# Kernel optimization log

Hardware: AMD Instinct MI355X
Metric: run time of the kernel (lower is better)

The kernel has to match this reference:

```python
import jax, jax.numpy as jnp
import numpy as np

NUM_GRAPHS = 1000


def _gine_conv(x, src, dst, edge_attr, w_e, b_e, w1, b1, w2, b2):
    # GINEConv (eps=0): out = nn(x + sum_{j->i} relu(x_j + lin_edge(e_ji)))
    e = edge_attr @ w_e + b_e                      # [E, F]
    m = jax.nn.relu(x[src] + e)                    # [E, F] per-edge message
    agg = jnp.zeros_like(x).at[dst].add(m)         # [N, F] scatter-add to targets
    h = x + agg
    h = jax.nn.relu(h @ w1 + b1)
    h = jax.nn.relu(h @ w2 + b2)
    return h


def _segment_softmax(scores, seg, num_segments):
    m = jax.ops.segment_max(scores, seg, num_segments=num_segments)
    z = jnp.exp(scores - m[seg])
    s = jax.ops.segment_sum(z, seg, num_segments=num_segments)
    return z / s[seg]


def setup_inputs() -> dict:
    key = jax.random.key(0)
    ks = jax.random.split(key, 16)
    N, E, F_IN, H, ED = 100000, 1600000, 9, 64, 1

    x = jax.random.normal(ks[0], (N, F_IN), dtype=jnp.float32)
    edge_index = jax.random.randint(ks[1], (2, E), 0, N, dtype=jnp.int32)
    edge_attr = jax.random.normal(ks[2], (E, ED), dtype=jnp.float32)
    batch = jnp.sort(jax.random.randint(ks[3], (N,), 0, NUM_GRAPHS, dtype=jnp.int32))
    B_total = jax.random.uniform(ks[4], (NUM_GRAPHS,), dtype=jnp.float32)

    def lin(k, fi, fo):
        k1, k2 = jax.random.split(k)
        bound = 1.0 / np.sqrt(fi)
        w = jax.random.uniform(k1, (fi, fo), minval=-bound, maxval=bound, dtype=jnp.float32)
        b = jax.random.uniform(k2, (fo,), minval=-bound, maxval=bound, dtype=jnp.float32)
        return w, b

    we1, be1 = lin(ks[5], ED, F_IN)    # conv1 edge projection -> in_channels
    w11, b11 = lin(ks[6], F_IN, H)
    w12, b12 = lin(ks[7], H, H)
    we2, be2 = lin(ks[8], ED, H)       # conv2 edge projection
    w21, b21 = lin(ks[9], H, H)
    w22, b22 = lin(ks[10], H, H)
    wr1, br1 = lin(ks[11], H, H // 2)
    wr2, br2 = lin(ks[12], H // 2, 1)

    return {"x": x, "edge_index": edge_index, "edge_attr": edge_attr,
            "batch": batch, "B_total": B_total,
            "we1": we1, "be1": be1, "w11": w11, "b11": b11, "w12": w12, "b12": b12,
            "we2": we2, "be2": be2, "w21": w21, "b21": b21, "w22": w22, "b22": b22,
            "wr1": wr1, "br1": br1, "wr2": wr2, "br2": br2}


def reference(x, edge_index, edge_attr, batch, B_total,
              we1, be1, w11, b11, w12, b12,
              we2, be2, w21, b21, w22, b22,
              wr1, br1, wr2, br2):
    src, dst = edge_index[0], edge_index[1]
    h = _gine_conv(x, src, dst, edge_attr, we1, be1, w11, b11, w12, b12)
    h = _gine_conv(h, src, dst, edge_attr, we2, be2, w21, b21, w22, b22)
    raw = (jax.nn.relu(h @ wr1 + br1) @ wr2 + br2)[:, 0]   # [N]
    alloc_probs = _segment_softmax(raw, batch, NUM_GRAPHS)
    return alloc_probs * B_total[batch]
```

## Files before the change

### kernel.cpp

```cpp
#include <hip/hip_runtime.h>
#include <float.h>

__global__ void deg_rank_kernel(const int* __restrict__ dst, int* __restrict__ deg,
                                int* __restrict__ rank, int E) {
  int j = blockIdx.x * blockDim.x + threadIdx.x;
  if (j < E) rank[j] = atomicAdd(&deg[dst[j]], 1);
}

__global__ void scan_pass1(const int* __restrict__ deg, int* __restrict__ blocksum, int N) {
  __shared__ int sdata[1024];
  int i = blockIdx.x * 1024 + threadIdx.x;
  sdata[threadIdx.x] = (i < N) ? deg[i] : 0;
  __syncthreads();
  for (int s = 512; s > 0; s >>= 1) {
    if (threadIdx.x < s) sdata[threadIdx.x] += sdata[threadIdx.x + s];
    __syncthreads();
  }
  if (threadIdx.x == 0) blocksum[blockIdx.x] = sdata[0];
}

__global__ void scan_pass2(int* __restrict__ blocksum, int nb) {
  __shared__ int sdata[1024];
  int t = threadIdx.x;
  sdata[t] = (t < nb) ? blocksum[t] : 0;
  __syncthreads();
  if (t == 0) {
    int run = 0;
    for (int i = 0; i < nb; ++i) { int v = sdata[i]; sdata[i] = run; run += v; }
  }
  __syncthreads();
  if (t < nb) blocksum[t] = sdata[t];
}

__global__ void scan_pass3(const int* __restrict__ deg, const int* __restrict__ blocksum,
                           int* __restrict__ rowptr, int N, int E) {
  __shared__ int sdata[1024];
  int i = blockIdx.x * 1024 + threadIdx.x;
  int v = (i < N) ? deg[i] : 0;
  sdata[threadIdx.x] = v;
  __syncthreads();
  for (int off = 1; off < 1024; off <<= 1) {
    int t = (threadIdx.x >= off) ? sdata[threadIdx.x - off] : 0;
    __syncthreads();
    sdata[threadIdx.x] += t;
    __syncthreads();
  }
  if (i < N) rowptr[i] = blocksum[blockIdx.x] + sdata[threadIdx.x] - v;
  if (i == 0) rowptr[N] = E;
}

__global__ void scatter_kernel(const int* __restrict__ dst, const int* __restrict__ rank,
                               const int* __restrict__ rowptr,
                               const int* __restrict__ src, const float* __restrict__ ea,
                               int2* __restrict__ epack, int E) {
  int j = blockIdx.x * blockDim.x + threadIdx.x;
  if (j >= E) return;
  int pos = rowptr[dst[j]] + rank[j];
  epack[pos] = make_int2(src[j], __float_as_int(ea[j]));
}

__global__ void __launch_bounds__(256, 8) gather1_kernel(
    const float* __restrict__ x, const int* __restrict__ rowptr,
    const int2* __restrict__ epack,
    const float* __restrict__ we1, const float* __restrict__ be1,
    float* __restrict__ xin, int N) {
  int i = blockIdx.x * blockDim.x + threadIdx.x;
  if (i >= N) return;
  float we[9], be[9];
#pragma unroll
  for (int f = 0; f < 9; ++f) { we[f] = we1[f]; be[f] = be1[f]; }
  float acc[9];
#pragma unroll
  for (int f = 0; f < 9; ++f) acc[f] = 0.0f;

  int p0 = rowptr[i], p1 = rowptr[i + 1];
  int p = p0;
  for (; p + 1 < p1; p += 2) {
    int2 e0 = epack[p], e1 = epack[p + 1];
    float a0 = __int_as_float(e0.y), a1 = __int_as_float(e1.y);
    float r0[9], r1[9];
#pragma unroll
    for (int f = 0; f < 9; ++f) r0[f] = x[(size_t)e0.x * 9 + f];
#pragma unroll
    for (int f = 0; f < 9; ++f) r1[f] = x[(size_t)e1.x * 9 + f];
#pragma unroll
    for (int f = 0; f < 9; ++f) {
      acc[f] += fmaxf(fmaf(a0, we[f], be[f]) + r0[f], 0.0f);
      acc[f] += fmaxf(fmaf(a1, we[f], be[f]) + r1[f], 0.0f);
    }
  }
  for (; p < p1; ++p) {
    int2 e = epack[p];
    float a = __int_as_float(e.y);
#pragma unroll
    for (int f = 0; f < 9; ++f)
      acc[f] += fmaxf(fmaf(a, we[f], be[f]) + x[(size_t)e.x * 9 + f], 0.0f);
  }
#pragma unroll
  for (int f = 0; f < 9; ++f) xin[(size_t)i * 9 + f] = x[(size_t)i * 9 + f] + acc[f];
}

__global__ void __launch_bounds__(256, 3) node1_mlp(
    const float* __restrict__ xin,
    const float* __restrict__ w11, const float* __restrict__ b11,
    const float* __restrict__ w12, const float* __restrict__ b12,
    float* __restrict__ h1t, int N) {
  __shared__ float sW1[9 * 64];
  __shared__ float sB1[64];
  __shared__ float sW2[64 * 64];
  __shared__ float sB2[64];
  for (int t = threadIdx.x; t < 9 * 64; t += blockDim.x) sW1[t] = w11[t];
  for (int t = threadIdx.x; t < 64; t += blockDim.x) { sB1[t] = b11[t]; sB2[t] = b12[t]; }
  for (int t = threadIdx.x; t < 64 * 64; t += blockDim.x) sW2[t] = w12[t];
  __syncthreads();
  int i = blockIdx.x * blockDim.x + threadIdx.x;
  if (i >= N) return;
  float xv[9];
#pragma unroll
  for (int k = 0; k < 9; ++k) xv[k] = xin[(size_t)i * 9 + k];
  float t1[64];
#pragma unroll
  for (int o = 0; o < 64; ++o) {
    float a = sB1[o];
#pragma unroll
    for (int k = 0; k < 9; ++k) a = fmaf(xv[k], sW1[k * 64 + o], a);
    t1[o] = fmaxf(a, 0.0f);
  }
  for (int o = 0; o < 64; ++o) {
    float a = sB2[o];
#pragma unroll
    for (int k = 0; k < 64; ++k) a = fmaf(t1[k], sW2[k * 64 + o], a);
    h1t[(size_t)o * N + i] = fmaxf(a, 0.0f);
  }
}

__global__ void __launch_bounds__(256) pack_kernel(
    const float* __restrict__ h1t, unsigned short* __restrict__ h1b, int N) {
  __shared__ unsigned short tile[64][72];
  int i0 = blockIdx.x * 64;
  int l = threadIdx.x & 63;
  int q = threadIdx.x >> 6;
  int node = i0 + l;
#pragma unroll
  for (int it = 0; it < 16; ++it) {
    int o = it * 4 + q;
    float v = (node < N) ? h1t[(size_t)o * N + node] : 0.0f;
    unsigned u = __float_as_uint(v);
    tile[l][o] = (unsigned short)((u + 0x7FFFu + ((u >> 16) & 1u)) >> 16);
  }
  __syncthreads();
#pragma unroll
  for (int it = 0; it < 4; ++it) {
    int idx = it * 256 + threadIdx.x;
    int r = idx >> 4;
    int c = idx & 15;
    if (i0 + r < N) {
      const unsigned short* tp = &tile[r][c * 4];
      uint2 v;
      v.x = (unsigned)tp[0] | ((unsigned)tp[1] << 16);
      v.y = (unsigned)tp[2] | ((unsigned)tp[3] << 16);
      *(uint2*)(h1b + (size_t)(i0 + r) * 64 + c * 4) = v;
    }
  }
}

__device__ __forceinline__ float4 bf4_to_f4(uint2 u) {
  float4 r;
  r.x = __uint_as_float(u.x << 16);
  r.y = __uint_as_float(u.x & 0xFFFF0000u);
  r.z = __uint_as_float(u.y << 16);
  r.w = __uint_as_float(u.y & 0xFFFF0000u);
  return r;
}

__global__ void __launch_bounds__(256, 8) gather2_kernel(
    const unsigned short* __restrict__ h1b, const int* __restrict__ rowptr,
    const int2* __restrict__ epack,
    const float* __restrict__ we2, const float* __restrict__ be2,
    float* __restrict__ agg2, int N) {
  int wid = threadIdx.x >> 6;
  int lane = threadIdx.x & 63;
  int g = lane >> 4;
  int l = lane & 15;
  int i = blockIdx.x * 4 + wid;
  if (i >= N) return;

  float4 we_l = *(const float4*)(we2 + 4 * l);
  float4 be_l = *(const float4*)(be2 + 4 * l);
  float4 acc = make_float4(0.f, 0.f, 0.f, 0.f);

  int p0 = rowptr[i], p1 = rowptr[i + 1];
  int p = p0 + g;
  for (; p + 4 < p1; p += 8) {
    int2 e0 = epack[p], e1 = epack[p + 4];
    float a0 = __int_as_float(e0.y), a1 = __int_as_float(e1.y);
    float4 h0 = bf4_to_f4(*(const uint2*)(h1b + (size_t)e0.x * 64 + 4 * l));
    float4 hv = bf4_to_f4(*(const uint2*)(h1b + (size_t)e1.x * 64 + 4 * l));
    acc.x += fmaxf(fmaf(a0, we_l.x, be_l.x) + h0.x, 0.f);
    acc.y += fmaxf(fmaf(a0, we_l.y, be_l.y) + h0.y, 0.f);
    acc.z += fmaxf(fmaf(a0, we_l.z, be_l.z) + h0.z, 0.f);
    acc.w += fmaxf(fmaf(a0, we_l.w, be_l.w) + h0.w, 0.f);
    acc.x += fmaxf(fmaf(a1, we_l.x, be_l.x) + hv.x, 0.f);
    acc.y += fmaxf(fmaf(a1, we_l.y, be_l.y) + hv.y, 0.f);
    acc.z += fmaxf(fmaf(a1, we_l.z, be_l.z) + hv.z, 0.f);
    acc.w += fmaxf(fmaf(a1, we_l.w, be_l.w) + hv.w, 0.f);
  }
  for (; p < p1; p += 4) {
    int2 e = epack[p];
    float a = __int_as_float(e.y);
    float4 h = bf4_to_f4(*(const uint2*)(h1b + (size_t)e.x * 64 + 4 * l));
    acc.x += fmaxf(fmaf(a, we_l.x, be_l.x) + h.x, 0.f);
    acc.y += fmaxf(fmaf(a, we_l.y, be_l.y) + h.y, 0.f);
    acc.z += fmaxf(fmaf(a, we_l.z, be_l.z) + h.z, 0.f);
    acc.w += fmaxf(fmaf(a, we_l.w, be_l.w) + h.w, 0.f);
  }
#pragma unroll
  for (int off = 16; off <= 32; off <<= 1) {
    acc.x += __shfl_xor(acc.x, off);
    acc.y += __shfl_xor(acc.y, off);
    acc.z += __shfl_xor(acc.z, off);
    acc.w += __shfl_xor(acc.w, off);
  }
  if (g == 0) {
    float4 hs = bf4_to_f4(*(const uint2*)(h1b + (size_t)i * 64 + 4 * l));
    acc.x += hs.x; acc.y += hs.y; acc.z += hs.z; acc.w += hs.w;
    *(float4*)(agg2 + (size_t)i * 64 + 4 * l) = acc;
  }
}

__global__ void __launch_bounds__(256, 2) node2_kernel(
    const float* __restrict__ agg2,
    const float* __restrict__ w21, const float* __restrict__ b21,
    const float* __restrict__ w22, const float* __restrict__ b22,
    const float* __restrict__ wr1, const float* __restrict__ br1,
    const float* __restrict__ wr2, const float* __restrict__ br2,
    float* __restrict__ raw, int N) {
  __shared__ float sW1t[64 * 64];
  __shared__ float sW2t[64 * 64];
  __shared__ float sWr1t[32 * 64];
  __shared__ float sB1[64];
  __shared__ float sB2[64];
  __shared__ float sBr1[32];
  __shared__ float sWr2[32];
  __shared__ float sBr2;
  for (int t = threadIdx.x; t < 64 * 64; t += blockDim.x) {
    int o = t >> 6, k = t & 63;
    sW1t[t] = w21[k * 64 + o];
    sW2t[t] = w22[k * 64 + o];
  }
  for (int t = threadIdx.x; t < 32 * 64; t += blockDim.x) {
    int o = t >> 6, k = t & 63;
    sWr1t[t] = wr1[k * 32 + o];
  }
  for (int t = threadIdx.x; t < 64; t += blockDim.x) { sB1[t] = b21[t]; sB2[t] = b22[t]; }
  for (int t = threadIdx.x; t < 32; t += blockDim.x) { sBr1[t] = br1[t]; sWr2[t] = wr2[t]; }
  if (threadIdx.x == 0) sBr2 = br2[0];
  __syncthreads();
  int i = blockIdx.x * blockDim.x + threadIdx.x;
  if (i >= N) return;
  float hin[64];
#pragma unroll
  for (int k = 0; k < 64; k += 4) {
    float4 v = *(const float4*)(agg2 + (size_t)i * 64 + k);
    hin[k] = v.x; hin[k + 1] = v.y; hin[k + 2] = v.z; hin[k + 3] = v.w;
  }
  float a1[64];
#pragma unroll
  for (int o = 0; o < 64; ++o) {
    float acc = sB1[o];
#pragma unroll
    for (int k = 0; k < 64; k += 4) {
      float4 wv = *(const float4*)(sW1t + o * 64 + k);
      acc = fmaf(hin[k], wv.x, acc);
      acc = fmaf(hin[k + 1], wv.y, acc);
      acc = fmaf(hin[k + 2], wv.z, acc);
      acc = fmaf(hin[k + 3], wv.w, acc);
    }
    a1[o] = fmaxf(acc, 0.0f);
  }
  float a2[64];
#pragma unroll
  for (int o = 0; o < 64; ++o) {
    float acc = sB2[o];
#pragma unroll
    for (int k = 0; k < 64; k += 4) {
      float4 wv = *(const float4*)(sW2t + o * 64 + k);
      acc = fmaf(a1[k], wv.x, acc);
      acc = fmaf(a1[k + 1], wv.y, acc);
      acc = fmaf(a1[k + 2], wv.z, acc);
      acc = fmaf(a1[k + 3], wv.w, acc);
    }
    a2[o] = fmaxf(acc, 0.0f);
  }
  float r[32];
#pragma unroll
  for (int o = 0; o < 32; ++o) {
    float acc = sBr1[o];
#pragma unroll
    for (int k = 0; k < 64; k += 4) {
      float4 wv = *(const float4*)(sWr1t + o * 64 + k);
      acc = fmaf(a2[k], wv.x, acc);
      acc = fmaf(a2[k + 1], wv.y, acc);
      acc = fmaf(a2[k + 2], wv.z, acc);
      acc = fmaf(a2[k + 3], wv.w, acc);
    }
    r[o] = fmaxf(acc, 0.0f);
  }
  float acc = sBr2;
#pragma unroll
  for (int k = 0; k < 32; ++k) acc = fmaf(r[k], sWr2[k], acc);
  raw[i] = acc;
}

__device__ __forceinline__ int lowerb(const int* __restrict__ a, int n, int key) {
  int lo = 0, hi = n;
  while (lo < hi) { int mid = (lo + hi) >> 1; if (a[mid] < key) lo = mid + 1; else hi = mid; }
  return lo;
}

__global__ void segsoftmax_kernel(const float* __restrict__ raw, const int* __restrict__ batch,
                                  const float* __restrict__ Btot, float* __restrict__ out, int N) {
  __shared__ float sred[256];
  int g = blockIdx.x;
  int tid = threadIdx.x;
  int start = lowerb(batch, N, g);
  int end = lowerb(batch, N, g + 1);
  if (start >= end) return;

  float m = -FLT_MAX;
  for (int i = start + tid; i < end; i += 256) m = fmaxf(m, raw[i]);
  sred[tid] = m;
  __syncthreads();
  for (int s = 128; s > 0; s >>= 1) {
    if (tid < s) sred[tid] = fmaxf(sred[tid], sred[tid + s]);
    __syncthreads();
  }
  m = sred[0];
  __syncthreads();

  float sum = 0.0f;
  for (int i = start + tid; i < end; i += 256) sum += expf(raw[i] - m);
  sred[tid] = sum;
  __syncthreads();
  for (int s = 128; s > 0; s >>= 1) {
    if (tid < s) sred[tid] += sred[tid + s];
    __syncthreads();
  }
  float scale = Btot[g] / sred[0];

  for (int i = start + tid; i < end; i += 256) out[i] = expf(raw[i] - m) * scale;
}

extern "C" void kernel_launch(void* const* d_in, const int* in_sizes, int n_in,
                              void* d_out, int out_size, void* d_ws, size_t ws_size,
                              hipStream_t stream) {
  const float* x     = (const float*)d_in[0];
  const int* eidx    = (const int*)d_in[1];
  const float* eattr = (const float*)d_in[2];
  const int* batch   = (const int*)d_in[3];
  const float* Btot  = (const float*)d_in[4];
  const float* we1 = (const float*)d_in[5];
  const float* be1 = (const float*)d_in[6];
  const float* w11 = (const float*)d_in[7];
  const float* b11 = (const float*)d_in[8];
  const float* w12 = (const float*)d_in[9];
  const float* b12 = (const float*)d_in[10];
  const float* we2 = (const float*)d_in[11];
  const float* be2 = (const float*)d_in[12];
  const float* w21 = (const float*)d_in[13];
  const float* b21 = (const float*)d_in[14];
  const float* w22 = (const float*)d_in[15];
  const float* b22 = (const float*)d_in[16];
  const float* wr1 = (const float*)d_in[17];
  const float* br1 = (const float*)d_in[18];
  const float* wr2 = (const float*)d_in[19];
  const float* br2 = (const float*)d_in[20];

  const int N  = in_sizes[0] / 9;
  const int E  = in_sizes[2];
  const int NG = in_sizes[4];
  const int* src = eidx;
  const int* dst = eidx + E;

  const int NB = (N + 1023) / 1024;

  char* w = (char*)d_ws;
  int*   deg    = (int*)w;                 w += (size_t)N * 4;
  int*   rowptr = (int*)w;                 w += (size_t)(N + 1) * 4;
  int*   blocksum = (int*)w;               w += (size_t)1024 * 4;
  int*   rank   = (int*)w;                 w += (size_t)E * 4;
  int2*  epack  = (int2*)w;                w += (size_t)E * 8;
  float* h1t    = (float*)w;               w += (size_t)N * 64 * 4;
  unsigned short* h1b = (unsigned short*)w; w += (size_t)N * 64 * 2;
  float* agg2   = (float*)w;               w += (size_t)N * 64 * 4;
  float* raw    = (float*)w;               w += (size_t)N * 4;
  float* xin = agg2;

  hipMemsetAsync(deg, 0, (size_t)N * 4, stream);

  dim3 blk(256);
  dim3 egrid((E + 255) / 256);
  dim3 ngrid((N + 255) / 256);

  deg_rank_kernel<<<egrid, blk, 0, stream>>>(dst, deg, rank, E);
  scan_pass1<<<dim3(NB), dim3(1024), 0, stream>>>(deg, blocksum, N);
  scan_pass2<<<dim3(1), dim3(1024), 0, stream>>>(blocksum, NB);
  scan_pass3<<<dim3(NB), dim3(1024), 0, stream>>>(deg, blocksum, rowptr, N, E);
  scatter_kernel<<<egrid, blk, 0, stream>>>(dst, rank, rowptr, src, eattr, epack, E);

  gather1_kernel<<<ngrid, blk, 0, stream>>>(x, rowptr, epack, we1, be1, xin, N);
  node1_mlp<<<ngrid, blk, 0, stream>>>(xin, w11, b11, w12, b12, h1t, N);
  pack_kernel<<<dim3((N + 63) / 64), blk, 0, stream>>>(h1t, h1b, N);

  dim3 l2grid((N + 3) / 4);
  gather2_kernel<<<l2grid, blk, 0, stream>>>(h1b, rowptr, epack, we2, be2, agg2, N);
  node2_kernel<<<ngrid, blk, 0, stream>>>(agg2, w21, b21, w22, b22,
                                          wr1, br1, wr2, br2, raw, N);

  segsoftmax_kernel<<<dim3(NG), blk, 0, stream>>>(raw, batch, Btot, (float*)d_out, N);
}
```

Before: 320.6 us.

## Fuse bf16 packing into node1 MLP and rebalance node2 grid

```diff
diff --git a/kernel.cpp b/kernel.cpp
--- a/kernel.cpp
+++ b/kernel.cpp
@@ -104,53 +104,52 @@
     const float* __restrict__ xin,
     const float* __restrict__ w11, const float* __restrict__ b11,
     const float* __restrict__ w12, const float* __restrict__ b12,
-    float* __restrict__ h1t, int N) {
+    unsigned short* __restrict__ h1b, int N) {
   __shared__ float sW1[9 * 64];
   __shared__ float sB1[64];
-  __shared__ float sW2[64 * 64];
+  __shared__ float sW2t[64 * 64];
   __shared__ float sB2[64];
+  __shared__ unsigned short tile[256][66];
   for (int t = threadIdx.x; t < 9 * 64; t += blockDim.x) sW1[t] = w11[t];
+  for (int t = threadIdx.x; t < 64 * 64; t += blockDim.x) {
+    int o = t >> 6, k = t & 63;
+    sW2t[t] = w12[k * 64 + o];
+  }
   for (int t = threadIdx.x; t < 64; t += blockDim.x) { sB1[t] = b11[t]; sB2[t] = b12[t]; }
-  for (int t = threadIdx.x; t < 64 * 64; t += blockDim.x) sW2[t] = w12[t];
-  __syncthreads();
-  int i = blockIdx.x * blockDim.x + threadIdx.x;
-  if (i >= N) return;
-  float xv[9];
-#pragma unroll
-  for (int k = 0; k < 9; ++k) xv[k] = xin[(size_t)i * 9 + k];
-  float t1[64];
-#pragma unroll
-  for (int o = 0; o < 64; ++o) {
-    float a = sB1[o];
-#pragma unroll
-    for (int k = 0; k < 9; ++k) a = fmaf(xv[k], sW1[k * 64 + o], a);
-    t1[o] = fmaxf(a, 0.0f);
-  }
-  for (int o = 0; o < 64; ++o) {
-    float a = sB2[o];
-#pragma unroll
-    for (int k = 0; k < 64; ++k) a = fmaf(t1[k], sW2[k * 64 + o], a);
-    h1t[(size_t)o * N + i] = fmaxf(a, 0.0f);
-  }
-}
-
-__global__ void __launch_bounds__(256) pack_kernel(
-    const float* __restrict__ h1t, unsigned short* __restrict__ h1b, int N) {
-  __shared__ unsigned short tile[64][72];
-  int i0 = blockIdx.x * 64;
-  int l = threadIdx.x & 63;
-  int q = threadIdx.x >> 6;
-  int node = i0 + l;
+  __syncthreads();
+  int i0 = blockIdx.x * 256;
+  int i = i0 + threadIdx.x;
+  if (i < N) {
+    float xv[9];
+#pragma unroll
+    for (int k = 0; k < 9; ++k) xv[k] = xin[(size_t)i * 9 + k];
+    float t1[64];
+#pragma unroll
+    for (int o = 0; o < 64; ++o) {
+      float a = sB1[o];
+#pragma unroll
+      for (int k = 0; k < 9; ++k) a = fmaf(xv[k], sW1[k * 64 + o], a);
+      t1[o] = fmaxf(a, 0.0f);
+    }
+#pragma unroll
+    for (int o = 0; o < 64; ++o) {
+      float a = sB2[o];
+#pragma unroll
+      for (int k = 0; k < 64; k += 4) {
+        float4 wv = *(const float4*)(sW2t + o * 64 + k);
+        a = fmaf(t1[k], wv.x, a);
+        a = fmaf(t1[k + 1], wv.y, a);
+        a = fmaf(t1[k + 2], wv.z, a);
+        a = fmaf(t1[k + 3], wv.w, a);
+      }
+      float v = fmaxf(a, 0.0f);
+      unsigned u = __float_as_uint(v);
+      tile[threadIdx.x][o] = (unsigned short)((u + 0x7FFFu + ((u >> 16) & 1u)) >> 16);
+    }
+  }
+  __syncthreads();
 #pragma unroll
   for (int it = 0; it < 16; ++it) {
-    int o = it * 4 + q;
-    float v = (node < N) ? h1t[(size_t)o * N + node] : 0.0f;
-    unsigned u = __float_as_uint(v);
-    tile[l][o] = (unsigned short)((u + 0x7FFFu + ((u >> 16) & 1u)) >> 16);
-  }
-  __syncthreads();
-#pragma unroll
-  for (int it = 0; it < 4; ++it) {
     int idx = it * 256 + threadIdx.x;
     int r = idx >> 4;
     int c = idx & 15;
@@ -234,7 +233,7 @@
     const float* __restrict__ w22, const float* __restrict__ b22,
     const float* __restrict__ wr1, const float* __restrict__ br1,
     const float* __restrict__ wr2, const float* __restrict__ br2,
-    float* __restrict__ raw, int N) {
+    float* __restrict__ raw, int N, int chunk) {
   __shared__ float sW1t[64 * 64];
   __shared__ float sW2t[64 * 64];
   __shared__ float sWr1t[32 * 64];
@@ -256,8 +255,8 @@
   for (int t = threadIdx.x; t < 32; t += blockDim.x) { sBr1[t] = br1[t]; sWr2[t] = wr2[t]; }
   if (threadIdx.x == 0) sBr2 = br2[0];
   __syncthreads();
-  int i = blockIdx.x * blockDim.x + threadIdx.x;
-  if (i >= N) return;
+  int i = blockIdx.x * chunk + threadIdx.x;
+  if ((int)threadIdx.x >= chunk || i >= N) return;
   float hin[64];
 #pragma unroll
   for (int k = 0; k < 64; k += 4) {
@@ -390,7 +389,6 @@
   int*   blocksum = (int*)w;               w += (size_t)1024 * 4;
   int*   rank   = (int*)w;                 w += (size_t)E * 4;
   int2*  epack  = (int2*)w;                w += (size_t)E * 8;
-  float* h1t    = (float*)w;               w += (size_t)N * 64 * 4;
   unsigned short* h1b = (unsigned short*)w; w += (size_t)N * 64 * 2;
   float* agg2   = (float*)w;               w += (size_t)N * 64 * 4;
   float* raw    = (float*)w;               w += (size_t)N * 4;
@@ -409,13 +407,14 @@
   scatter_kernel<<<egrid, blk, 0, stream>>>(dst, rank, rowptr, src, eattr, epack, E);
 
   gather1_kernel<<<ngrid, blk, 0, stream>>>(x, rowptr, epack, we1, be1, xin, N);
-  node1_mlp<<<ngrid, blk, 0, stream>>>(xin, w11, b11, w12, b12, h1t, N);
-  pack_kernel<<<dim3((N + 63) / 64), blk, 0, stream>>>(h1t, h1b, N);
+  node1_mlp<<<ngrid, blk, 0, stream>>>(xin, w11, b11, w12, b12, h1b, N);
 
   dim3 l2grid((N + 3) / 4);
   gather2_kernel<<<l2grid, blk, 0, stream>>>(h1b, rowptr, epack, we2, be2, agg2, N);
-  node2_kernel<<<ngrid, blk, 0, stream>>>(agg2, w21, b21, w22, b22,
-                                          wr1, br1, wr2, br2, raw, N);
+  const int N2B = 512;
+  const int chunk = (N + N2B - 1) / N2B;
+  node2_kernel<<<dim3(N2B), blk, 0, stream>>>(agg2, w21, b21, w22, b22,
+                                              wr1, br1, wr2, br2, raw, N, chunk);
 
   segsoftmax_kernel<<<dim3(NG), blk, 0, stream>>>(raw, batch, Btot, (float*)d_out, N);
 }
```

Measured after the change: 300.0 us. 6.4% less time.
